# Performance work log

Hardware: AMD Instinct MI355X
Metric: run time of the kernel (lower is better)

Reference implementation:

```python
import jax, jax.numpy as jnp
import numpy as np


def setup_inputs() -> dict:
    key = jax.random.key(0)
    k1, k2, k3 = jax.random.split(key, 3)
    B, C_IN, C_OUT, R, K = 4, 64, 64, 64, 3
    x = jax.random.normal(k1, (B, C_IN, R, R, R), dtype=jnp.float32)
    # per-voxel nonzero test |x|.sum(channel) != 0 used by the module)
    keep = jax.random.uniform(k2, (B, 1, R, R, R)) < 0.3
    x = x * keep.astype(jnp.float32)
    weight = jax.random.normal(k3, (C_OUT, C_IN, K, K, K), dtype=jnp.float32)
    return {"x": x, "weight": weight}


def reference(x, weight):
    # The torch module gathers a k^3 neighborhood at every nonzero input voxel,
    # contracts with the (unflipped) weight, and scatters to the same voxel.
    # This is exactly cross-correlation (torch conv semantics) with SAME padding,
    # masked to voxels where the input is nonzero across channels.
    K = weight.shape[-1]
    pad_l = K // 2
    pad_r = K - 1 - pad_l
    out = jax.lax.conv_general_dilated(
        x, weight,
        window_strides=(1, 1, 1),
        padding=[(pad_l, pad_r)] * 3,
        dimension_numbers=("NCDHW", "OIDHW", "NCDHW"),
    )  # [B, C_out, D, H, W]
    mask = (jnp.abs(x).sum(axis=1, keepdims=True) != 0)  # [B,1,D,H,W]
    return out * mask.astype(out.dtype)
```

## Files before the change

kernel.cpp:

```cpp
#include <hip/hip_runtime.h>
#include <stdint.h>


#define R3 262144
#define NVOX (4 * R3)
#define P  66
#define PS (66 * 66)
#define PB (66 * 66 * 66)
#define WSW_ELEMS (27 * 2 * 4 * 64 * 8)
#define CAP (NVOX / 2)

typedef __attribute__((ext_vector_type(4))) float f32x4;
typedef __attribute__((ext_vector_type(8))) short short8;

static __device__ inline unsigned short f2bf(float f) {
    union { float f; unsigned u; } v; v.f = f;
    unsigned u = v.u;
    return (unsigned short)((u + 0x7fffu + ((u >> 16) & 1u)) >> 16);
}

static __device__ __forceinline__ void gload16(const void* g, void* l) {
    __builtin_amdgcn_global_load_lds(
        (const __attribute__((address_space(1))) unsigned int*)g,
        (__attribute__((address_space(3))) unsigned int*)l, 16, 0, 0);
}

__global__ void __launch_bounds__(256) prep_misc(const float* __restrict__ w,
                                                 unsigned short* __restrict__ wsw,
                                                 uint4* __restrict__ xt4) {
    int idx = blockIdx.x * 256 + threadIdx.x;
    if (idx < 4 * PB) {
        int b = idx / PB;
        int rp = idx - b * PB;
        int z = rp / PS; rp -= z * PS;
        int y = rp / P;  int xx = rp - y * P;
        if (z == 0 || z == 65 || y == 0 || y == 65 || xx == 0 || xx == 65) {
            uint4 zz = {0, 0, 0, 0};
            uint4* d = xt4 + (size_t)idx * 8;
#pragma unroll
            for (int k = 0; k < 8; ++k) d[k] = zz;
        }
    }
    if (idx < WSW_ELEMS) {
        int e = idx;
        int j    = e & 7;
        int lane = (e >> 3) & 63;
        int nt   = (e >> 9) & 3;
        int kc   = (e >> 11) & 1;
        int tap  = e >> 12;
        int co = nt * 16 + (lane & 15);
        int ci = kc * 32 + ((lane >> 4) * 8) + j;
        wsw[e] = f2bf(w[(co * 64 + ci) * 27 + tap]);
    }
}

__global__ void __launch_bounds__(256) xprep(const float* __restrict__ x,
                                             unsigned int* __restrict__ xt_u32,
                                             int* __restrict__ list,
                                             int* __restrict__ pos,
                                             int* __restrict__ count) {
    __shared__ unsigned int lds[256 * 36];
    __shared__ unsigned int wcnt[4], wbase[4], bbase;
    int t = threadIdx.x;
    int v = blockIdx.x * 256 + t;
    int b = v >> 18;
    int s = v & (R3 - 1);
    const float* xb = x + (size_t)b * (64 * R3) + s;
    bool active = false;
    unsigned int pk[32];
#pragma unroll
    for (int c2 = 0; c2 < 32; ++c2) {
        float f0 = xb[(size_t)(2 * c2) * R3];
        float f1 = xb[(size_t)(2 * c2 + 1) * R3];
        active |= (f0 != 0.f) | (f1 != 0.f);
        pk[c2] = (unsigned)f2bf(f0) | ((unsigned)f2bf(f1) << 16);
    }
#pragma unroll
    for (int k = 0; k < 8; ++k) {
        uint4 q = { pk[4 * k], pk[4 * k + 1], pk[4 * k + 2], pk[4 * k + 3] };
        *(uint4*)&lds[t * 36 + 4 * k] = q;
    }
    __syncthreads();
    int s0 = (blockIdx.x * 256) & (R3 - 1);
    int z0 = s0 >> 12;
    int y0 = (s0 >> 6) & 63;
    size_t rowbase = ((size_t)b * PB + (size_t)(z0 + 1) * PS + (size_t)(y0 + 1) * P + 1) * 32;
#pragma unroll
    for (int i = 0; i < 8; ++i) {
        int g4 = i * 256 + t;
        int vox = g4 >> 3;
        int col = (g4 & 7) * 4;
        uint4 val = *(const uint4*)&lds[vox * 36 + col];
        int r = vox >> 6;
        int xc = vox & 63;
        *(uint4*)&xt_u32[rowbase + (size_t)r * (P * 32) + (size_t)xc * 32 + col] = val;
    }
    int lane = t & 63, w = t >> 6;
    unsigned long long bal = __ballot(active);
    if (lane == 0) wcnt[w] = (unsigned)__popcll(bal);
    __syncthreads();
    if (t == 0) {
        unsigned tot = 0;
        for (int i = 0; i < 4; ++i) { wbase[i] = tot; tot += wcnt[i]; }
        bbase = (unsigned)atomicAdd(count, (int)tot);
    }
    __syncthreads();
    int p = -1;
    if (active) {
        unsigned pp = bbase + wbase[w] + (unsigned)__popcll(bal & ((1ULL << lane) - 1ULL));
        list[pp] = v;
        p = (int)pp;
    }
    pos[v] = p;
}

#define STAGE(tap, buf) do {                                                       \
    const int dz_ = (tap) / 9 - 1, dy_ = ((tap) / 3) % 3 - 1, dx_ = (tap) % 3 - 1; \
    const ptrdiff_t dlt_ = (ptrdiff_t)(dz_ * PS + dy_ * P + dx_) * 128;            \
    _Pragma("unroll")                                                              \
    for (int i_ = 0; i_ < 4; ++i_)                                                 \
        gload16(asrc[i_] + dlt_, &Ab[buf][t * 16 + i_ * 8192]);                    \
    gload16(wswb + (size_t)(tap) * 8192 + t * 16, &Bb[buf][t * 16]);               \
} while (0)

__global__ void __launch_bounds__(512) sconv_gemm(const unsigned char* __restrict__ xt,
                                                  const unsigned char* __restrict__ wswb,
                                                  const int* __restrict__ list,
                                                  const int* __restrict__ count_p,
                                                  float* __restrict__ out,
                                                  float* __restrict__ compact,
                                                  int use_compact) {
    __shared__ __align__(16) unsigned char Ab[2][32768];
    __shared__ __align__(16) unsigned char Bb[2][8192];
    int count = *count_p;
    int nt_act = (count + 255) >> 8;
    int bid = blockIdx.x;
    if (bid >= nt_act) return;
    int qd = nt_act >> 3, rd = nt_act & 7;
    int xcd = bid & 7, ixx = bid >> 3;
    int tile = (xcd < rd ? xcd * (qd + 1) : rd * (qd + 1) + (xcd - rd) * qd) + ixx;
    int base = tile * 256;
    int t = threadIdx.x;

    const unsigned char* asrc[4];
    {
        int seg = t & 7;
        int r0 = t >> 3;
        int off = (seg * 16) ^ ((r0 & 7) << 4);
#pragma unroll
        for (int i = 0; i < 4; ++i) {
            int gi = base + r0 + 64 * i;
            int vid = (gi < count) ? list[gi] : 0;
            if (vid < 0) vid = 0;
            int bb = vid >> 18, sp = vid & (R3 - 1);
            int vz = sp >> 12, vy = (sp >> 6) & 63, vx = sp & 63;
            size_t pvox = (size_t)bb * PB + (size_t)(vz + 1) * PS + (size_t)(vy + 1) * P + (vx + 1);
            asrc[i] = xt + pvox * 128 + off;
        }
    }

    int lane = t & 63, w = t >> 6;
    int cl = lane & 15;
    int hi16 = (lane >> 4) * 16;
    int aswz = (cl & 7) << 4;
    int aoff[2][2];
#pragma unroll
    for (int m = 0; m < 2; ++m)
#pragma unroll
        for (int kc = 0; kc < 2; ++kc)
            aoff[m][kc] = (w * 32 + m * 16 + cl) * 128 + ((kc * 64 + hi16) ^ aswz);
    int boff[2][4];
#pragma unroll
    for (int kc = 0; kc < 2; ++kc)
#pragma unroll
        for (int n = 0; n < 4; ++n)
            boff[kc][n] = ((kc * 4 + n) * 64 + lane) * 16;

    f32x4 acc[2][4] = {};

    STAGE(0, 0);
#pragma unroll
    for (int tap = 0; tap < 27; ++tap) {
        const int cur = tap & 1;
        asm volatile("s_waitcnt vmcnt(0)" ::: "memory");
        asm volatile("s_barrier" ::: "memory");
        if (tap < 26) { STAGE(tap + 1, cur ^ 1); }
#pragma unroll
        for (int kc = 0; kc < 2; ++kc) {
            short8 a0 = *(const short8*)&Ab[cur][aoff[0][kc]];
            short8 a1 = *(const short8*)&Ab[cur][aoff[1][kc]];
#pragma unroll
            for (int n = 0; n < 4; ++n) {
                short8 bf = *(const short8*)&Bb[cur][boff[kc][n]];
                acc[0][n] = __builtin_amdgcn_mfma_f32_16x16x32_bf16(a0, bf, acc[0][n], 0, 0, 0);
                acc[1][n] = __builtin_amdgcn_mfma_f32_16x16x32_bf16(a1, bf, acc[1][n], 0, 0, 0);
            }
        }
        asm volatile("s_waitcnt lgkmcnt(0)" ::: "memory");
    }

    int q = lane >> 4;
    if (use_compact) {
#pragma unroll
        for (int m = 0; m < 2; ++m) {
#pragma unroll
            for (int rg = 0; rg < 4; ++rg) {
                int row = w * 32 + m * 16 + q * 4 + rg;
                int gi = base + row;
                if (gi < count && gi < CAP) {
#pragma unroll
                    for (int n = 0; n < 4; ++n)
                        compact[(size_t)gi * 64 + n * 16 + cl] = acc[m][n][rg];
                }
            }
        }
    } else {
#pragma unroll
        for (int m = 0; m < 2; ++m) {
#pragma unroll
            for (int rg = 0; rg < 4; ++rg) {
                int row = w * 32 + m * 16 + q * 4 + rg;
                int gi = base + row;
                if (gi < count) {
                    int vv = list[gi];
                    int bb2 = vv >> 18;
                    int sp = vv & (R3 - 1);
                    float* op = out + (size_t)(bb2 * 64 + cl) * R3 + sp;
#pragma unroll
                    for (int n = 0; n < 4; ++n)
                        op[(size_t)(n * 16) * R3] = acc[m][n][rg];
                }
            }
        }
    }
}

__global__ void __launch_bounds__(256) finalize(const uint4* __restrict__ compact4,
                                                const int* __restrict__ pos,
                                                float* __restrict__ out) {
    int t = threadIdx.x;
    int vb = blockIdx.x * 256;
    int b = vb >> 18;
    int sp0 = vb & (R3 - 1);
    int q = pos[vb + t];
    bool act = (unsigned)q < (unsigned)CAP;
    const uint4* src = compact4 + (size_t)(act ? q : 0) * 16;
    uint4 r[16];
#pragma unroll
    for (int s = 0; s < 16; ++s) {
        uint4 v = {0, 0, 0, 0};
        if (act) v = src[s];
        r[s] = v;
    }
    const float* rf = (const float*)r;
    float* ob = out + (size_t)b * 64 * R3 + sp0 + t;
#pragma unroll
    for (int co = 0; co < 64; ++co)
        ob[(size_t)co * R3] = rf[co];
}

__global__ void __launch_bounds__(64) fallback_conv(const float* __restrict__ x,
                                                    const float* __restrict__ wt,
                                                    float* __restrict__ out) {
    __shared__ float rowb[66];
    int bid = blockIdx.x;
    int y = bid & 63, z = (bid >> 6) & 63, co = (bid >> 12) & 63, b = bid >> 18;
    int t = threadIdx.x;
    float acc = 0.f;
    bool active = false;
    for (int ci = 0; ci < 64; ++ci) {
        const float* xp = x + ((size_t)(b * 64 + ci)) * R3;
        const float* wp = wt + ((size_t)(co * 64 + ci)) * 27;
        for (int dz = -1; dz <= 1; ++dz) {
            int nz = z + dz;
            bool okz = (unsigned)nz < 64u;
            for (int dy = -1; dy <= 1; ++dy) {
                int ny = y + dy;
                bool ok = okz && ((unsigned)ny < 64u);
                float v = ok ? xp[nz * 4096 + ny * 64 + t] : 0.f;
                rowb[t + 1] = v;
                if (t == 0) { rowb[0] = 0.f; rowb[65] = 0.f; }
                __syncthreads();
                if (dz == 0 && dy == 0) active |= (rowb[t + 1] != 0.f);
                const float* wq = wp + (dz + 1) * 9 + (dy + 1) * 3;
                acc += rowb[t] * wq[0] + rowb[t + 1] * wq[1] + rowb[t + 2] * wq[2];
                __syncthreads();
            }
        }
    }
    out[((size_t)(b * 64 + co)) * R3 + z * 4096 + y * 64 + t] = active ? acc : 0.f;
}

extern "C" void kernel_launch(void* const* d_in, const int* in_sizes, int n_in,
                              void* d_out, int out_size, void* d_ws, size_t ws_size,
                              hipStream_t stream) {
    const float* x = (const float*)d_in[0];
    const float* w = (const float*)d_in[1];
    float* out = (float*)d_out;

    const size_t XT_BYTES = (size_t)4 * PB * 128;
    const size_t LIST_OFF = XT_BYTES;
    const size_t POS_OFF  = LIST_OFF + (size_t)NVOX * 4;
    const size_t WSW_OFF  = POS_OFF + (size_t)NVOX * 4;
    const size_t CNT_OFF  = WSW_OFF + (size_t)WSW_ELEMS * 2;
    const size_t CMP_OFF  = (CNT_OFF + 256 + 255) & ~(size_t)255;
    const size_t NEED_S   = CMP_OFF;
    const size_t NEED_C   = CMP_OFF + (size_t)CAP * 64 * 4;

    if (ws_size < NEED_S) {
        fallback_conv<<<NVOX, 64, 0, stream>>>(x, w, out);
        return;
    }

    unsigned int*   xt   = (unsigned int*)d_ws;
    int*            list = (int*)((char*)d_ws + LIST_OFF);
    int*            pos  = (int*)((char*)d_ws + POS_OFF);
    unsigned short* wsw  = (unsigned short*)((char*)d_ws + WSW_OFF);
    int*            cnt  = (int*)((char*)d_ws + CNT_OFF);
    float*          cmp  = (float*)((char*)d_ws + CMP_OFF);
    int use_compact = (ws_size >= NEED_C) ? 1 : 0;

    hipMemsetAsync(cnt, 0, sizeof(int), stream);
    if (!use_compact)
        hipMemsetAsync(d_out, 0, (size_t)out_size * sizeof(float), stream);
    prep_misc<<<(4 * PB + 255) / 256, 256, 0, stream>>>(w, wsw, (uint4*)d_ws);
    xprep<<<NVOX / 256, 256, 0, stream>>>(x, xt, list, pos, cnt);
    sconv_gemm<<<NVOX / 256, 512, 0, stream>>>((const unsigned char*)xt,
                                               (const unsigned char*)wsw, list, cnt,
                                               out, cmp, use_compact);
    if (use_compact)
        finalize<<<NVOX / 256, 256, 0, stream>>>((const uint4*)cmp, pos, out);
}
```

Before: 648.6 us.

## Halve GEMM block to 256 threads with 64-row warp tiles and register-held weights

The sparse-conv GEMM block drops from 512 to 256 threads, so each wave now computes 64 rows (4x4 MFMA tiles) and reuses each B fragment across four A fragments. The weight tile is no longer staged through LDS. Each lane loads its B fragments straight from global memory into a double-buffered register array, which cuts LDS traffic and LDS size per block. The cost is higher register pressure (more accumulators plus the B registers), possibly lower occupancy, and global-load latency for B that the vmcnt wait now exposes.

```diff
diff --git a/kernel.cpp b/kernel.cpp
--- a/kernel.cpp
+++ b/kernel.cpp
@@ -118,20 +118,24 @@
     const int dz_ = (tap) / 9 - 1, dy_ = ((tap) / 3) % 3 - 1, dx_ = (tap) % 3 - 1; \
     const ptrdiff_t dlt_ = (ptrdiff_t)(dz_ * PS + dy_ * P + dx_) * 128;            \
     _Pragma("unroll")                                                              \
-    for (int i_ = 0; i_ < 4; ++i_)                                                 \
-        gload16(asrc[i_] + dlt_, &Ab[buf][t * 16 + i_ * 8192]);                    \
-    gload16(wswb + (size_t)(tap) * 8192 + t * 16, &Bb[buf][t * 16]);               \
+    for (int i_ = 0; i_ < 8; ++i_)                                                 \
+        gload16(asrc[i_] + dlt_, &Ab[buf][t * 16 + i_ * 4096]);                    \
 } while (0)
 
-__global__ void __launch_bounds__(512) sconv_gemm(const unsigned char* __restrict__ xt,
-                                                  const unsigned char* __restrict__ wswb,
-                                                  const int* __restrict__ list,
-                                                  const int* __restrict__ count_p,
-                                                  float* __restrict__ out,
-                                                  float* __restrict__ compact,
-                                                  int use_compact) {
+#define BLOAD(tap, st) do {                                                        \
+    _Pragma("unroll")                                                              \
+    for (int j_ = 0; j_ < 8; ++j_)                                                 \
+        breg[st][j_] = *(const short8*)(wswb + (size_t)(tap) * 8192 + boff[j_]);   \
+} while (0)
+
+__global__ void __launch_bounds__(256, 2) sconv_gemm(const unsigned char* __restrict__ xt,
+                                                     const unsigned char* __restrict__ wswb,
+                                                     const int* __restrict__ list,
+                                                     const int* __restrict__ count_p,
+                                                     float* __restrict__ out,
+                                                     float* __restrict__ compact,
+                                                     int use_compact) {
     __shared__ __align__(16) unsigned char Ab[2][32768];
-    __shared__ __align__(16) unsigned char Bb[2][8192];
     int count = *count_p;
     int nt_act = (count + 255) >> 8;
     int bid = blockIdx.x;
@@ -142,14 +146,14 @@
     int base = tile * 256;
     int t = threadIdx.x;
 
-    const unsigned char* asrc[4];
+    const unsigned char* asrc[8];
     {
         int seg = t & 7;
         int r0 = t >> 3;
         int off = (seg * 16) ^ ((r0 & 7) << 4);
 #pragma unroll
-        for (int i = 0; i < 4; ++i) {
-            int gi = base + r0 + 64 * i;
+        for (int i = 0; i < 8; ++i) {
+            int gi = base + r0 + 32 * i;
             int vid = (gi < count) ? list[gi] : 0;
             if (vid < 0) vid = 0;
             int bb = vid >> 18, sp = vid & (R3 - 1);
@@ -163,37 +167,40 @@
     int cl = lane & 15;
     int hi16 = (lane >> 4) * 16;
     int aswz = (cl & 7) << 4;
-    int aoff[2][2];
-#pragma unroll
-    for (int m = 0; m < 2; ++m)
+    int aoff[4][2];
+#pragma unroll
+    for (int m = 0; m < 4; ++m)
 #pragma unroll
         for (int kc = 0; kc < 2; ++kc)
-            aoff[m][kc] = (w * 32 + m * 16 + cl) * 128 + ((kc * 64 + hi16) ^ aswz);
-    int boff[2][4];
-#pragma unroll
-    for (int kc = 0; kc < 2; ++kc)
-#pragma unroll
-        for (int n = 0; n < 4; ++n)
-            boff[kc][n] = ((kc * 4 + n) * 64 + lane) * 16;
-
-    f32x4 acc[2][4] = {};
+            aoff[m][kc] = (w * 64 + m * 16 + cl) * 128 + ((kc * 64 + hi16) ^ aswz);
+    int boff[8];
+#pragma unroll
+    for (int j = 0; j < 8; ++j)
+        boff[j] = (j * 64 + lane) * 16;
+
+    f32x4 acc[4][4] = {};
+    short8 breg[2][8];
 
     STAGE(0, 0);
+    BLOAD(0, 0);
 #pragma unroll
     for (int tap = 0; tap < 27; ++tap) {
         const int cur = tap & 1;
         asm volatile("s_waitcnt vmcnt(0)" ::: "memory");
         asm volatile("s_barrier" ::: "memory");
-        if (tap < 26) { STAGE(tap + 1, cur ^ 1); }
+        if (tap < 26) { STAGE(tap + 1, cur ^ 1); BLOAD(tap + 1, cur ^ 1); }
 #pragma unroll
         for (int kc = 0; kc < 2; ++kc) {
-            short8 a0 = *(const short8*)&Ab[cur][aoff[0][kc]];
-            short8 a1 = *(const short8*)&Ab[cur][aoff[1][kc]];
+            short8 af[4];
+#pragma unroll
+            for (int m = 0; m < 4; ++m)
+                af[m] = *(const short8*)&Ab[cur][aoff[m][kc]];
 #pragma unroll
             for (int n = 0; n < 4; ++n) {
-                short8 bf = *(const short8*)&Bb[cur][boff[kc][n]];
-                acc[0][n] = __builtin_amdgcn_mfma_f32_16x16x32_bf16(a0, bf, acc[0][n], 0, 0, 0);
-                acc[1][n] = __builtin_amdgcn_mfma_f32_16x16x32_bf16(a1, bf, acc[1][n], 0, 0, 0);
+                short8 bf = breg[cur][kc * 4 + n];
+#pragma unroll
+                for (int m = 0; m < 4; ++m)
+                    acc[m][n] = __builtin_amdgcn_mfma_f32_16x16x32_bf16(af[m], bf, acc[m][n], 0, 0, 0);
             }
         }
         asm volatile("s_waitcnt lgkmcnt(0)" ::: "memory");
@@ -202,10 +209,10 @@
     int q = lane >> 4;
     if (use_compact) {
 #pragma unroll
-        for (int m = 0; m < 2; ++m) {
+        for (int m = 0; m < 4; ++m) {
 #pragma unroll
             for (int rg = 0; rg < 4; ++rg) {
-                int row = w * 32 + m * 16 + q * 4 + rg;
+                int row = w * 64 + m * 16 + q * 4 + rg;
                 int gi = base + row;
                 if (gi < count && gi < CAP) {
 #pragma unroll
@@ -216,10 +223,10 @@
         }
     } else {
 #pragma unroll
-        for (int m = 0; m < 2; ++m) {
+        for (int m = 0; m < 4; ++m) {
 #pragma unroll
             for (int rg = 0; rg < 4; ++rg) {
-                int row = w * 32 + m * 16 + q * 4 + rg;
+                int row = w * 64 + m * 16 + q * 4 + rg;
                 int gi = base + row;
                 if (gi < count) {
                     int vv = list[gi];
@@ -325,7 +332,7 @@
         hipMemsetAsync(d_out, 0, (size_t)out_size * sizeof(float), stream);
     prep_misc<<<(4 * PB + 255) / 256, 256, 0, stream>>>(w, wsw, (uint4*)d_ws);
     xprep<<<NVOX / 256, 256, 0, stream>>>(x, xt, list, pos, cnt);
-    sconv_gemm<<<NVOX / 256, 512, 0, stream>>>((const unsigned char*)xt,
+    sconv_gemm<<<NVOX / 256, 256, 0, stream>>>((const unsigned char*)xt,
                                                (const unsigned char*)wsw, list, cnt,
                                                out, cmp, use_compact);
     if (use_compact)
```

Measured after the change: 662.0 us. 1.02x slower.
